# Kernel tuning notes

Hardware: AMD Instinct MI355X
Metric: run time of the kernel (lower is better)

## Reference

```python
import jax, jax.numpy as jnp
import numpy as np

# OPT-1.3B attention, decode phase with paged KV cache
E = 2048      # embed_dim
H = 32        # num_heads
D = E // H    # head_dim = 64
S = 64        # num decoding sequences (q_len = 1 each)
L = 2048      # max context length per sequence
BS = 16       # cache block size (vLLM default)
BPS = L // BS # blocks per sequence = 128
NB = S * BPS  # total cache blocks = 8192


def setup_inputs() -> dict:
    key = jax.random.key(0)
    ks = jax.random.split(key, 6)
    hidden_states = jax.random.normal(ks[0], (S, E), jnp.float32) * 0.02
    wqkv = jax.random.normal(ks[1], (E, 3 * E), jnp.float32) * 0.02
    bqkv = jnp.zeros((3 * E,), jnp.float32)
    wout = jax.random.normal(ks[2], (E, E), jnp.float32) * 0.02
    bout = jnp.zeros((E,), jnp.float32)
    key_cache = jax.random.normal(ks[3], (NB, BS, H, D), jnp.float32)
    value_cache = jax.random.normal(ks[4], (NB, BS, H, D), jnp.float32)
    # each sequence owns BPS distinct cache blocks (non-contiguous in general)
    block_tables = jnp.arange(S * BPS, dtype=jnp.int32).reshape(S, BPS)
    context_lens = jax.random.randint(ks[5], (S,), L // 2, L + 1).astype(jnp.int32)
    return dict(hidden_states=hidden_states, wqkv=wqkv, bqkv=bqkv,
                wout=wout, bout=bout, key_cache=key_cache,
                value_cache=value_cache, block_tables=block_tables,
                context_lens=context_lens)


def reference(hidden_states, wqkv, bqkv, wout, bout,
              key_cache, value_cache, block_tables, context_lens):
    scale = 1.0 / np.sqrt(D).astype(np.float32)
    # fused QKV projection
    qkv = hidden_states @ wqkv + bqkv                    # [S, 3E]
    q, k, v = jnp.split(qkv, 3, axis=-1)
    q = q.reshape(S, H, D)
    k_new = k.reshape(S, 1, H, D)
    v_new = v.reshape(S, 1, H, D)
    # paged gather of the KV cache: [S, BPS, BS, H, D] -> [S, L, H, D]
    keys = key_cache[block_tables].reshape(S, L, H, D)
    vals = value_cache[block_tables].reshape(S, L, H, D)
    # decode step attends over cached context plus the current token
    keys = jnp.concatenate([keys, k_new], axis=1)        # [S, L+1, H, D]
    vals = jnp.concatenate([vals, v_new], axis=1)
    scores = jnp.einsum('shd,slhd->shl', q, keys) * scale
    pos = jnp.arange(L + 1)
    valid = (pos[None, :] < context_lens[:, None]) | (pos[None, :] == L)
    scores = jnp.where(valid[:, None, :], scores, jnp.float32(-1e30))
    probs = jax.nn.softmax(scores, axis=-1)              # [S, H, L+1]
    attn = jnp.einsum('shl,slhd->shd', probs, vals).reshape(S, E)
    # output projection
    return attn @ wout + bout
```

## Files before the change

### kernel.cpp

```cpp
#include <hip/hip_runtime.h>
#include <math.h>

#define S_ 64
#define E_ 2048
#define H_ 32
#define D_ 64
#define L_ 2048
#define BS_ 16
#define BPS_ 128
#define QKV_N (3 * E_)

__global__ __launch_bounds__(256) void gemm64(const float* __restrict__ A,
                                              const float* __restrict__ B,
                                              const float* __restrict__ bias,
                                              float* __restrict__ C,
                                              int K, int N) {
    __shared__ float As[64][32];
    const int t    = threadIdx.x;
    const int lane = t & 63;
    const int mg   = t >> 6;
    const int colbase = blockIdx.x * 128 + lane * 2;
    const int kchunk  = K / gridDim.y;
    const int ks      = blockIdx.y * kchunk;

    float2 acc[16];
    if (blockIdx.y == 0) {
        float2 bb = *(const float2*)(bias + colbase);
#pragma unroll
        for (int mm = 0; mm < 16; ++mm) acc[mm] = bb;
    } else {
#pragma unroll
        for (int mm = 0; mm < 16; ++mm) acc[mm] = make_float2(0.f, 0.f);
    }

    for (int k0 = ks; k0 < ks + kchunk; k0 += 32) {
        __syncthreads();
#pragma unroll
        for (int i = 0; i < 2; ++i) {
            int f4  = t + i * 256;
            int row = f4 >> 3, c4 = f4 & 7;
            *(float4*)&As[row][c4 * 4] =
                *(const float4*)(A + (size_t)row * K + k0 + c4 * 4);
        }
        __syncthreads();
#pragma unroll
        for (int kk = 0; kk < 32; kk += 4) {
            float2 b0 = *(const float2*)(B + (size_t)(k0 + kk + 0) * N + colbase);
            float2 b1 = *(const float2*)(B + (size_t)(k0 + kk + 1) * N + colbase);
            float2 b2 = *(const float2*)(B + (size_t)(k0 + kk + 2) * N + colbase);
            float2 b3 = *(const float2*)(B + (size_t)(k0 + kk + 3) * N + colbase);
#pragma unroll
            for (int mm = 0; mm < 16; ++mm) {
                float4 a = *(const float4*)&As[mg * 16 + mm][kk];
                acc[mm].x = fmaf(a.x, b0.x, acc[mm].x);
                acc[mm].y = fmaf(a.x, b0.y, acc[mm].y);
                acc[mm].x = fmaf(a.y, b1.x, acc[mm].x);
                acc[mm].y = fmaf(a.y, b1.y, acc[mm].y);
                acc[mm].x = fmaf(a.z, b2.x, acc[mm].x);
                acc[mm].y = fmaf(a.z, b2.y, acc[mm].y);
                acc[mm].x = fmaf(a.w, b3.x, acc[mm].x);
                acc[mm].y = fmaf(a.w, b3.y, acc[mm].y);
            }
        }
    }
#pragma unroll
    for (int mm = 0; mm < 16; ++mm) {
        float* cp = C + (size_t)(mg * 16 + mm) * N + colbase;
        atomicAdd(cp + 0, acc[mm].x);
        atomicAdd(cp + 1, acc[mm].y);
    }
}

__global__ __launch_bounds__(256, 6) void paged_attn(
        const float* __restrict__ qkv,
        const float* __restrict__ kcache,
        const float* __restrict__ vcache,
        const int* __restrict__ btab,
        const int* __restrict__ clens,
        float* __restrict__ attn) {
    const int bid  = blockIdx.x;
    const int s    = bid >> 5;
    const int h    = bid & 31;
    const int t    = threadIdx.x;
    const int w    = t >> 6;
    const int lane = t & 63;
    const int g    = lane >> 3;
    const int j    = lane & 7;
    const int ctx  = clens[s];
    const int nb   = (ctx + 15) >> 4;
    const float scale = 0.125f;

    const float* qp = qkv + (size_t)s * QKV_N + h * 64 + j * 8;
    const float4 q0 = *(const float4*)(qp);
    const float4 q1 = *(const float4*)(qp + 4);

    float m = -1e30f, l = 0.f;
    float4 a0 = make_float4(0.f, 0.f, 0.f, 0.f);
    float4 a1 = make_float4(0.f, 0.f, 0.f, 0.f);

    const int* bt   = btab + s * BPS_;
    const int  hoff = h * 64 + j * 8;

    for (int b = w; b < nb; b += 4) {
        const int blk = bt[b];
        const size_t blkbase = (size_t)blk * (BS_ * H_ * D_) + hoff;
#pragma unroll
        for (int half = 0; half < 2; ++half) {
            const size_t base = blkbase + (size_t)(half * 8 + g) * (H_ * D_);
            const float* kp = kcache + base;
            const float* vp = vcache + base;
            const float4 k0 = *(const float4*)(kp);
            const float4 k1 = *(const float4*)(kp + 4);
            const float4 v0 = *(const float4*)(vp);
            const float4 v1 = *(const float4*)(vp + 4);

            float part = q0.x * k0.x + q0.y * k0.y + q0.z * k0.z + q0.w * k0.w
                       + q1.x * k1.x + q1.y * k1.y + q1.z * k1.z + q1.w * k1.w;
            part += __shfl_xor(part, 1);
            part += __shfl_xor(part, 2);
            part += __shfl_xor(part, 4);

            const int tok = b * 16 + half * 8 + g;
            const float score = (tok < ctx) ? part * scale : -1e38f;
            const float nm = fmaxf(m, score);
            const float r  = __expf(m - nm);
            const float p  = __expf(score - nm);
            m = nm;
            l = fmaf(l, r, p);
            a0.x = fmaf(p, v0.x, a0.x * r);
            a0.y = fmaf(p, v0.y, a0.y * r);
            a0.z = fmaf(p, v0.z, a0.z * r);
            a0.w = fmaf(p, v0.w, a0.w * r);
            a1.x = fmaf(p, v1.x, a1.x * r);
            a1.y = fmaf(p, v1.y, a1.y * r);
            a1.z = fmaf(p, v1.z, a1.z * r);
            a1.w = fmaf(p, v1.w, a1.w * r);
        }
    }

#pragma unroll
    for (int msk = 8; msk <= 32; msk <<= 1) {
        float om = __shfl_xor(m, msk);
        float ol = __shfl_xor(l, msk);
        float nm = fmaxf(m, om);
        float ra = __expf(m - nm);
        float rb = __expf(om - nm);
        l = ra * l + rb * ol;
        a0.x = ra * a0.x + rb * __shfl_xor(a0.x, msk);
        a0.y = ra * a0.y + rb * __shfl_xor(a0.y, msk);
        a0.z = ra * a0.z + rb * __shfl_xor(a0.z, msk);
        a0.w = ra * a0.w + rb * __shfl_xor(a0.w, msk);
        a1.x = ra * a1.x + rb * __shfl_xor(a1.x, msk);
        a1.y = ra * a1.y + rb * __shfl_xor(a1.y, msk);
        a1.z = ra * a1.z + rb * __shfl_xor(a1.z, msk);
        a1.w = ra * a1.w + rb * __shfl_xor(a1.w, msk);
        m = nm;
    }

    if (w == 0) {
        const float* kn = qkv + (size_t)s * QKV_N + E_ + h * 64 + j * 8;
        const float* vn = qkv + (size_t)s * QKV_N + 2 * E_ + h * 64 + j * 8;
        const float4 k0 = *(const float4*)(kn);
        const float4 k1 = *(const float4*)(kn + 4);
        float part = q0.x * k0.x + q0.y * k0.y + q0.z * k0.z + q0.w * k0.w
                   + q1.x * k1.x + q1.y * k1.y + q1.z * k1.z + q1.w * k1.w;
        part += __shfl_xor(part, 1);
        part += __shfl_xor(part, 2);
        part += __shfl_xor(part, 4);
        const float score = part * scale;
        const float nm = fmaxf(m, score);
        const float r  = __expf(m - nm);
        const float p  = __expf(score - nm);
        l = fmaf(l, r, p);
        const float4 v0 = *(const float4*)(vn);
        const float4 v1 = *(const float4*)(vn + 4);
        a0.x = fmaf(p, v0.x, a0.x * r);
        a0.y = fmaf(p, v0.y, a0.y * r);
        a0.z = fmaf(p, v0.z, a0.z * r);
        a0.w = fmaf(p, v0.w, a0.w * r);
        a1.x = fmaf(p, v1.x, a1.x * r);
        a1.y = fmaf(p, v1.y, a1.y * r);
        a1.z = fmaf(p, v1.z, a1.z * r);
        a1.w = fmaf(p, v1.w, a1.w * r);
        m = nm;
    }

    __shared__ float lm[4], ll[4], la[4][64];
    if (g == 0) {
        *(float4*)&la[w][j * 8]     = a0;
        *(float4*)&la[w][j * 8 + 4] = a1;
    }
    if (lane == 0) { lm[w] = m; ll[w] = l; }
    __syncthreads();

    if (t < 64) {
        const int d = t;
        float M = fmaxf(fmaxf(lm[0], lm[1]), fmaxf(lm[2], lm[3]));
        float Lsum = 0.f, o = 0.f;
#pragma unroll
        for (int ww = 0; ww < 4; ++ww) {
            float f = __expf(lm[ww] - M);
            Lsum += f * ll[ww];
            o += f * la[ww][d];
        }
        attn[(size_t)s * E_ + h * 64 + d] = o / Lsum;
    }
}

extern "C" void kernel_launch(void* const* d_in, const int* in_sizes, int n_in,
                              void* d_out, int out_size, void* d_ws, size_t ws_size,
                              hipStream_t stream) {
    const float* hidden = (const float*)d_in[0];
    const float* wqkv   = (const float*)d_in[1];
    const float* bqkv   = (const float*)d_in[2];
    const float* wout   = (const float*)d_in[3];
    const float* bout   = (const float*)d_in[4];
    const float* kcache = (const float*)d_in[5];
    const float* vcache = (const float*)d_in[6];
    const int*   btab   = (const int*)d_in[7];
    const int*   clens  = (const int*)d_in[8];
    float* out = (float*)d_out;

    float* qkv     = (float*)d_ws;
    float* attnbuf = qkv + (size_t)S_ * QKV_N;

    hipMemsetAsync(qkv, 0, (size_t)S_ * QKV_N * sizeof(float), stream);
    hipMemsetAsync(out, 0, (size_t)S_ * E_ * sizeof(float), stream);

    gemm64<<<dim3(QKV_N / 128, 8), 256, 0, stream>>>(hidden, wqkv, bqkv, qkv,
                                                     E_, QKV_N);
    paged_attn<<<dim3(S_ * H_), 256, 0, stream>>>(qkv, kcache, vcache, btab,
                                                  clens, attnbuf);
    gemm64<<<dim3(E_ / 128, 16), 256, 0, stream>>>(attnbuf, wout, bout, out,
                                                   E_, E_);
}
```

Measured before the change: 405.3 us.

## Split paged attention into per-chunk partial kernel plus merge kernel

Replaces the single per-(sequence, head) attention block with a split-K style scheme. Each wavefront now handles one contiguous 256-token chunk and writes its partial max, sum and accumulator to workspace. A separate merge kernel combines the chunks and folds in the current token. This is meant to raise parallelism and give each wave contiguous block ranges, at the cost of an extra kernel launch and a round trip through global memory for the partials.

```diff
diff --git a/kernel.cpp b/kernel.cpp
--- a/kernel.cpp
+++ b/kernel.cpp
@@ -9,6 +9,9 @@
 #define BS_ 16
 #define BPS_ 128
 #define QKV_N (3 * E_)
+#define CHUNK_TOK 256
+#define CHUNK_BLKS 16
+#define MAXCH 8
 
 __global__ __launch_bounds__(256) void gemm64(const float* __restrict__ A,
                                               const float* __restrict__ B,
@@ -71,23 +74,27 @@
     }
 }
 
-__global__ __launch_bounds__(256, 6) void paged_attn(
+__global__ __launch_bounds__(128, 6) void attn_chunk(
         const float* __restrict__ qkv,
         const float* __restrict__ kcache,
         const float* __restrict__ vcache,
         const int* __restrict__ btab,
         const int* __restrict__ clens,
-        float* __restrict__ attn) {
-    const int bid  = blockIdx.x;
-    const int s    = bid >> 5;
-    const int h    = bid & 31;
-    const int t    = threadIdx.x;
-    const int w    = t >> 6;
+        float* __restrict__ ml,
+        float* __restrict__ pacc) {
+    const int bid = blockIdx.x;
+    const int sh  = bid >> 2;
+    const int t   = threadIdx.x;
+    const int w   = t >> 6;
+    const int c   = ((bid & 3) << 1) | w;
+    const int s   = sh >> 5;
+    const int h   = sh & 31;
+    const int ctx = clens[s];
+    if (c * CHUNK_TOK >= ctx) return;
+
     const int lane = t & 63;
     const int g    = lane >> 3;
     const int j    = lane & 7;
-    const int ctx  = clens[s];
-    const int nb   = (ctx + 15) >> 4;
     const float scale = 0.125f;
 
     const float* qp = qkv + (size_t)s * QKV_N + h * 64 + j * 8;
@@ -100,8 +107,9 @@
 
     const int* bt   = btab + s * BPS_;
     const int  hoff = h * 64 + j * 8;
-
-    for (int b = w; b < nb; b += 4) {
+    const int  bend = min(c * CHUNK_BLKS + CHUNK_BLKS, (ctx + 15) >> 4);
+
+    for (int b = c * CHUNK_BLKS; b < bend; ++b) {
         const int blk = bt[b];
         const size_t blkbase = (size_t)blk * (BS_ * H_ * D_) + hoff;
 #pragma unroll
@@ -157,54 +165,58 @@
         m = nm;
     }
 
-    if (w == 0) {
-        const float* kn = qkv + (size_t)s * QKV_N + E_ + h * 64 + j * 8;
-        const float* vn = qkv + (size_t)s * QKV_N + 2 * E_ + h * 64 + j * 8;
-        const float4 k0 = *(const float4*)(kn);
-        const float4 k1 = *(const float4*)(kn + 4);
-        float part = q0.x * k0.x + q0.y * k0.y + q0.z * k0.z + q0.w * k0.w
-                   + q1.x * k1.x + q1.y * k1.y + q1.z * k1.z + q1.w * k1.w;
-        part += __shfl_xor(part, 1);
-        part += __shfl_xor(part, 2);
-        part += __shfl_xor(part, 4);
-        const float score = part * scale;
-        const float nm = fmaxf(m, score);
-        const float r  = __expf(m - nm);
-        const float p  = __expf(score - nm);
-        l = fmaf(l, r, p);
-        const float4 v0 = *(const float4*)(vn);
-        const float4 v1 = *(const float4*)(vn + 4);
-        a0.x = fmaf(p, v0.x, a0.x * r);
-        a0.y = fmaf(p, v0.y, a0.y * r);
-        a0.z = fmaf(p, v0.z, a0.z * r);
-        a0.w = fmaf(p, v0.w, a0.w * r);
-        a1.x = fmaf(p, v1.x, a1.x * r);
-        a1.y = fmaf(p, v1.y, a1.y * r);
-        a1.z = fmaf(p, v1.z, a1.z * r);
-        a1.w = fmaf(p, v1.w, a1.w * r);
-        m = nm;
-    }
-
-    __shared__ float lm[4], ll[4], la[4][64];
+    const int slot = sh * MAXCH + c;
     if (g == 0) {
-        *(float4*)&la[w][j * 8]     = a0;
-        *(float4*)&la[w][j * 8 + 4] = a1;
-    }
-    if (lane == 0) { lm[w] = m; ll[w] = l; }
-    __syncthreads();
-
-    if (t < 64) {
-        const int d = t;
-        float M = fmaxf(fmaxf(lm[0], lm[1]), fmaxf(lm[2], lm[3]));
-        float Lsum = 0.f, o = 0.f;
-#pragma unroll
-        for (int ww = 0; ww < 4; ++ww) {
-            float f = __expf(lm[ww] - M);
-            Lsum += f * ll[ww];
-            o += f * la[ww][d];
-        }
-        attn[(size_t)s * E_ + h * 64 + d] = o / Lsum;
-    }
+        *(float4*)&pacc[(size_t)slot * 64 + j * 8]     = a0;
+        *(float4*)&pacc[(size_t)slot * 64 + j * 8 + 4] = a1;
+    }
+    if (lane == 0) {
+        ml[slot * 2 + 0] = m;
+        ml[slot * 2 + 1] = l;
+    }
+}
+
+__global__ __launch_bounds__(64) void attn_merge(
+        const float* __restrict__ qkv,
+        const int* __restrict__ clens,
+        const float* __restrict__ ml,
+        const float* __restrict__ pacc,
+        float* __restrict__ attn) {
+    const int sh = blockIdx.x;
+    const int s  = sh >> 5;
+    const int h  = sh & 31;
+    const int d  = threadIdx.x;
+    const int ctx = clens[s];
+    const int nch = (ctx + CHUNK_TOK - 1) / CHUNK_TOK;
+
+    float M = -1e30f, L = 0.f, O = 0.f;
+    for (int c = 0; c < nch; ++c) {
+        const int slot = sh * MAXCH + c;
+        const float mc = ml[slot * 2 + 0];
+        const float lc = ml[slot * 2 + 1];
+        const float oc = pacc[(size_t)slot * 64 + d];
+        const float nm = fmaxf(M, mc);
+        const float ra = __expf(M - nm);
+        const float rb = __expf(mc - nm);
+        O = O * ra + oc * rb;
+        L = L * ra + lc * rb;
+        M = nm;
+    }
+
+    const float qd = qkv[(size_t)s * QKV_N + h * 64 + d];
+    const float kd = qkv[(size_t)s * QKV_N + E_ + h * 64 + d];
+    float part = qd * kd;
+#pragma unroll
+    for (int msk = 1; msk <= 32; msk <<= 1) part += __shfl_xor(part, msk);
+    const float score = part * 0.125f;
+    const float nm = fmaxf(M, score);
+    const float r  = __expf(M - nm);
+    const float p  = __expf(score - nm);
+    const float vd = qkv[(size_t)s * QKV_N + 2 * E_ + h * 64 + d];
+    O = O * r + p * vd;
+    L = L * r + p;
+
+    attn[(size_t)s * E_ + h * 64 + d] = O / L;
 }
 
 extern "C" void kernel_launch(void* const* d_in, const int* in_sizes, int n_in,
@@ -223,14 +235,17 @@
 
     float* qkv     = (float*)d_ws;
     float* attnbuf = qkv + (size_t)S_ * QKV_N;
+    float* ml      = attnbuf + (size_t)S_ * E_;
+    float* pacc    = ml + (size_t)S_ * H_ * MAXCH * 2;
 
     hipMemsetAsync(qkv, 0, (size_t)S_ * QKV_N * sizeof(float), stream);
     hipMemsetAsync(out, 0, (size_t)S_ * E_ * sizeof(float), stream);
 
     gemm64<<<dim3(QKV_N / 128, 8), 256, 0, stream>>>(hidden, wqkv, bqkv, qkv,
                                                      E_, QKV_N);
-    paged_attn<<<dim3(S_ * H_), 256, 0, stream>>>(qkv, kcache, vcache, btab,
-                                                  clens, attnbuf);
+    attn_chunk<<<dim3(S_ * H_ * 4), 128, 0, stream>>>(qkv, kcache, vcache,
+                                                      btab, clens, ml, pacc);
+    attn_merge<<<dim3(S_ * H_), 64, 0, stream>>>(qkv, clens, ml, pacc, attnbuf);
     gemm64<<<dim3(E_ / 128, 16), 256, 0, stream>>>(attnbuf, wout, bout, out,
                                                    E_, E_);
 }
```

New measurement: 466.0 us. +15.0%, slower.
